# Performance work log

Measured on AMD Instinct MI355X. Metric: run time of the kernel, lower is better.

Reference implementation:

```python
import jax, jax.numpy as jnp
import numpy as np

SLOT_DIM = 64
EPS_SHIFT = 1e-6


def _mlp(x, Ws, bs):
    for i in range(len(Ws) - 1):
        x = jax.nn.relu(x @ Ws[i] + bs[i])
    return x @ Ws[-1] + bs[-1]


def setup_inputs() -> dict:
    key = jax.random.key(0)
    ks = jax.random.split(key, 16)
    B, C, H, W = 2, 64, 64, 64
    Q = 65536  # 256x256 output queries
    feat = jax.random.normal(ks[0], (B, C, H, W), jnp.float32)
    coord = jax.random.uniform(ks[1], (B, Q, 2), jnp.float32, -1.0, 1.0)
    cell = jnp.full((B, Q, 2), 2.0 / 256.0, jnp.float32)
    in_dim = C * 9 + 2 + 2  # unfolded feat + rel_coord + rel_cell
    dims = [in_dim, 256, 256, 256, 256, 3]
    params = {}
    for i in range(5):
        params[f"W{i}"] = jax.random.normal(ks[2 + i], (dims[i], dims[i + 1]), jnp.float32) * (1.0 / np.sqrt(dims[i]))
        params[f"b{i}"] = jnp.zeros((dims[i + 1],), jnp.float32)
    return {"feat": feat, "coord": coord, "cell": cell, **params}


def reference(feat, coord, cell, W0, b0, W1, b1, W2, b2, W3, b3, W4, b4):
    Ws = [W0, W1, W2, W3, W4]
    bs = [b0, b1, b2, b3, b4]
    B, C, H, W = feat.shape
    slot_flat = feat[:, -SLOT_DIM:].reshape(B, SLOT_DIM, H * W)
    # F.unfold(feat, 3, padding=1): channel order c*9 + ky*3 + kx
    pad = jnp.pad(feat, ((0, 0), (0, 0), (1, 1), (1, 1)))
    feat_unf = jnp.stack(
        [pad[:, :, ky:ky + H, kx:kx + W] for ky in range(3) for kx in range(3)],
        axis=2).reshape(B, C * 9, H * W)
    rx = 1.0 / H  # 2/H/2
    ry = 1.0 / W
    preds, slots = [], []
    for vx in (-1.0, 1.0):
        for vy in (-1.0, 1.0):
            cy = jnp.clip(coord[..., 0] + vx * rx + EPS_SHIFT, -1 + 1e-6, 1 - 1e-6)
            cx = jnp.clip(coord[..., 1] + vy * ry + EPS_SHIFT, -1 + 1e-6, 1 - 1e-6)
            # nearest grid_sample, align_corners=False: pix = (c+1)*N/2 - 0.5
            iy = jnp.clip(jnp.round((cy + 1.0) * H / 2.0 - 0.5), 0, H - 1).astype(jnp.int32)
            ix = jnp.clip(jnp.round((cx + 1.0) * W / 2.0 - 0.5), 0, W - 1).astype(jnp.int32)
            idx = iy * W + ix  # [B, Q]
            q_feat = jnp.take_along_axis(feat_unf, idx[:, None, :], axis=2).transpose(0, 2, 1)  # [B,Q,C*9]
            q_slot = jnp.take_along_axis(slot_flat, idx[:, None, :], axis=2).transpose(0, 2, 1)  # [B,Q,S]
            # make_coord pixel centers at sampled indices
            qc_y = -1.0 + (2.0 * iy.astype(coord.dtype) + 1.0) / H
            qc_x = -1.0 + (2.0 * ix.astype(coord.dtype) + 1.0) / W
            rel_y = (coord[..., 0] - qc_y) * H
            rel_x = (coord[..., 1] - qc_x) * W
            rel_cell = cell * jnp.asarray([H, W], coord.dtype)
            inp = jnp.concatenate([q_feat, rel_y[..., None], rel_x[..., None], rel_cell], axis=-1)
            preds.append(_mlp(inp, Ws, bs))  # [B,Q,3]
            slots.append(q_slot)
    # self-attention ensemble weighting
    slots = jnp.stack(slots, axis=-1)  # [B,Q,S,4]
    normed = slots / jnp.linalg.norm(slots, axis=-2, keepdims=True)
    n_shift = slots.shape[-1]
    attn = jnp.einsum('bqsi,bqsj->bqij', normed, normed) / SLOT_DIM  # mean over slot dim
    mask = 1.0 - jnp.eye(n_shift, dtype=attn.dtype)
    w = jnp.mean(attn * mask[None, None], axis=-1)  # [B,Q,4]
    w = w / jnp.sum(w, axis=-1, keepdims=True)
    ret = preds[0] * w[..., 0:1]
    for i in range(1, n_shift):
        ret = ret + preds[i] * w[..., i:i + 1]
    return ret
```

## Files before the change

### kernel.cpp

```cpp
#include <hip/hip_runtime.h>
#include <hip/hip_bf16.h>
#include <hip/hip_fp16.h>

typedef _Float16 f16x8 __attribute__((ext_vector_type(8)));
typedef _Float16 h2 __attribute__((ext_vector_type(2)));
typedef float f32x4 __attribute__((ext_vector_type(4)));

#define OFF_FEAT_T   0u
#define OFF_FEAT_H   (2u*1024*1024)
#define OFF_G        (3u*1024*1024)
#define OFF_WP1      (7u*1024*1024)
#define OFF_WP2      (OFF_WP1 + 131072u)
#define OFF_WP3      (OFF_WP2 + 131072u)
#define OFF_WP4      (OFF_WP3 + 131072u)
#define OFF_W0PT     (OFF_WP4 + 8192u)
#define OFF_W0E      (OFF_W0PT + 294912u)

__device__ __forceinline__ unsigned short f2h(float v) {
  return __builtin_bit_cast(unsigned short, (_Float16)v);
}
__device__ __forceinline__ unsigned pk2(float a, float b) {
  auto p = __builtin_amdgcn_cvt_pkrtz(a, b);
  return __builtin_bit_cast(unsigned, p);
}
__device__ __forceinline__ void block_sync() {
  asm volatile("s_waitcnt lgkmcnt(0)" ::: "memory");
  __builtin_amdgcn_s_barrier();
}

__global__ __launch_bounds__(256) void prep_kernel(
    const float* __restrict__ feat, const float* __restrict__ W0,
    const float* __restrict__ b0,
    const float* __restrict__ W1, const float* __restrict__ W2,
    const float* __restrict__ W3, const float* __restrict__ W4,
    char* __restrict__ ws)
{
  int flat = blockIdx.x * 256 + threadIdx.x;
  if (flat < 524288) {
    int c = flat & 63, x = (flat >> 6) & 63, y = (flat >> 12) & 63, b = flat >> 18;
    float f = feat[(((b*64 + c) << 6) + y)*64 + x];
    ((float*)(ws + OFF_FEAT_T))[flat] = f;
    ((unsigned short*)(ws + OFF_FEAT_H))[flat] = f2h(f);
    return;
  }
  int e = flat - 524288;
  if (e >= 44544) return;
  unsigned short o[8];
  char* dst;
  if (e < 24576) {
    int layer = e >> 13, ee = e & 8191;
    const float* Wsrc = layer == 0 ? W1 : (layer == 1 ? W2 : W3);
    int lane = ee & 63, nb = (ee >> 6) & 15, kk = ee >> 10;
    int n = nb*16 + (lane & 15), kb = kk*32 + ((lane >> 4) << 3);
    #pragma unroll
    for (int j = 0; j < 8; ++j) o[j] = f2h(Wsrc[(kb + j)*256 + n]);
    dst = ws + OFF_WP1 + layer*131072 + ee*16;
  } else if (e < 25088) {
    int ee = e - 24576;
    int lane = ee & 63, kk = ee >> 6;
    int n = lane & 15, kb = kk*32 + ((lane >> 4) << 3);
    #pragma unroll
    for (int j = 0; j < 8; ++j)
      o[j] = (n < 3) ? f2h(W4[(kb + j)*3 + n]) : (unsigned short)0;
    dst = ws + OFF_WP4 + ee*16;
  } else if (e < 43520) {
    int ee = e - 25088;
    int lane = ee & 63, nb = (ee >> 6) & 15, kk = ee >> 10;
    int n = nb*16 + (lane & 15), kb = kk*32 + ((lane >> 4) << 3);
    #pragma unroll
    for (int j = 0; j < 8; ++j) {
      int kp = kb + j, tap = kp >> 6, ch = kp & 63;
      o[j] = f2h(W0[(ch*9 + tap)*256 + n]);
    }
    dst = ws + OFF_W0PT + ee*16;
  } else {
    int ee = e - 43520;
    int lane = ee & 63, nb = ee >> 6;
    int n = nb*16 + (lane & 15), kb = (lane >> 4) << 3;
    #pragma unroll
    for (int j = 0; j < 8; ++j) {
      int k = kb + j;
      float v = (k < 4) ? W0[(576 + k)*256 + n] : (k == 4 ? b0[n] : 0.0f);
      o[j] = f2h(v);
    }
    dst = ws + OFF_W0E + ee*16;
  }
  uint4 v;
  v.x = (unsigned)o[0] | ((unsigned)o[1] << 16);
  v.y = (unsigned)o[2] | ((unsigned)o[3] << 16);
  v.z = (unsigned)o[4] | ((unsigned)o[5] << 16);
  v.w = (unsigned)o[6] | ((unsigned)o[7] << 16);
  *(uint4*)dst = v;
}

__global__ __launch_bounds__(256) void g_kernel(char* __restrict__ ws)
{
  __shared__ __align__(16) char As[32 * 1152];
  int t = threadIdx.x, lane = t & 63, w = t >> 6;
  int bid = blockIdx.x, b = bid >> 7, rb = bid & 127;
  int y = rb >> 1, x0 = (rb & 1) << 5;
  {
    int r = t >> 3, cq = t & 7;
    const unsigned short* fh = (const unsigned short*)(ws + OFF_FEAT_H);
    #pragma unroll
    for (int tap = 0; tap < 9; ++tap) {
      int dy = tap/3 - 1, dx = tap%3 - 1;
      int sy = y + dy, sx = x0 + r + dx;
      uint4 v = {0,0,0,0};
      if (sy >= 0 && sy < 64 && sx >= 0 && sx < 64)
        v = *(const uint4*)(fh + (((((b << 6) + sy) << 6) + sx) << 6) + (cq << 3));
      *(uint4*)(As + r*1152 + ((tap*128 + cq*16) ^ ((r & 7) << 4))) = v;
    }
  }
  __syncthreads();
  const f32x4 vzero = {0.f, 0.f, 0.f, 0.f};
  f32x4 acc[4][2];
  #pragma unroll
  for (int i = 0; i < 4; ++i)
    #pragma unroll
    for (int j = 0; j < 2; ++j) acc[i][j] = vzero;
  const unsigned short* wp0 = (const unsigned short*)(ws + OFF_W0PT);
  int lr = lane & 15, lg = lane >> 4;
  #pragma unroll
  for (int kk = 0; kk < 18; ++kk) {
    f16x8 a[4], bf[2];
    #pragma unroll
    for (int mf = 0; mf < 4; ++mf)
      a[mf] = *(const f16x8*)(wp0 + (((kk*16 + w*4 + mf)*64 + lane) << 3));
    #pragma unroll
    for (int nf = 0; nf < 2; ++nf) {
      int row = nf*16 + lr;
      bf[nf] = *(const f16x8*)(As + row*1152 + ((kk*64 + (lg << 4)) ^ ((row & 7) << 4)));
    }
    #pragma unroll
    for (int mf = 0; mf < 4; ++mf)
      #pragma unroll
      for (int nf = 0; nf < 2; ++nf)
        acc[mf][nf] = __builtin_amdgcn_mfma_f32_16x16x32_f16(a[mf], bf[nf], acc[mf][nf], 0, 0, 0);
  }
  unsigned short* gp = (unsigned short*)(ws + OFF_G);
  #pragma unroll
  for (int mf = 0; mf < 4; ++mf)
    #pragma unroll
    for (int nf = 0; nf < 2; ++nf) {
      int col = (w << 6) + mf*16 + (lg << 2);
      int p = (y << 6) + x0 + nf*16 + lr;
      uint2 ov;
      ov.x = pk2(acc[mf][nf][0], acc[mf][nf][1]);
      ov.y = pk2(acc[mf][nf][2], acc[mf][nf][3]);
      *(uint2*)(gp + ((((b << 12) + p) << 8) + col)) = ov;
    }
}

__device__ __forceinline__ void hidden_layer(const char* src, char* dst,
                                             const unsigned short* wp,
                                             const float* bias,
                                             int lane, int wc,
                                             const f16x8* apre)
{
  int lr = lane & 15, lg = lane >> 4;
  f32x4 acc[4][4];
  #pragma unroll
  for (int mf = 0; mf < 4; ++mf) {
    float4 bv = *(const float4*)(bias + (wc << 6) + (mf << 4) + (lg << 2));
    f32x4 bi = {bv.x, bv.y, bv.z, bv.w};
    #pragma unroll
    for (int nf = 0; nf < 4; ++nf) acc[mf][nf] = bi;
  }
  #pragma unroll
  for (int kk = 0; kk < 8; ++kk) {
    f16x8 a[4], bb[4];
    #pragma unroll
    for (int mf = 0; mf < 4; ++mf)
      a[mf] = (kk == 0) ? apre[mf]
            : *(const f16x8*)(wp + (((kk*16 + wc*4 + mf)*64 + lane) << 3));
    #pragma unroll
    for (int nf = 0; nf < 4; ++nf) {
      int row = (nf << 4) + lr;
      bb[nf] = *(const f16x8*)(src + row*512 + ((((kk << 2) + lg) ^ (row & 31)) << 4));
    }
    #pragma unroll
    for (int mf = 0; mf < 4; ++mf)
      #pragma unroll
      for (int nf = 0; nf < 4; ++nf)
        acc[mf][nf] = __builtin_amdgcn_mfma_f32_16x16x32_f16(a[mf], bb[nf], acc[mf][nf], 0, 0, 0);
  }
  #pragma unroll
  for (int mf = 0; mf < 4; ++mf) {
    int unit = (wc << 3) + (mf << 1) + (lg >> 1);
    int half8 = (lg & 1) << 3;
    #pragma unroll
    for (int nf = 0; nf < 4; ++nf) {
      int row = (nf << 4) + lr;
      float v0 = fmaxf(acc[mf][nf][0], 0.f);
      float v1 = fmaxf(acc[mf][nf][1], 0.f);
      float v2 = fmaxf(acc[mf][nf][2], 0.f);
      float v3 = fmaxf(acc[mf][nf][3], 0.f);
      uint2 ov;
      ov.x = pk2(v0, v1);
      ov.y = pk2(v2, v3);
      *(uint2*)(dst + row*512 + (((unit ^ (row & 31)) << 4) + half8)) = ov;
    }
  }
}

__global__ __launch_bounds__(256) void main_kernel(
    const float* __restrict__ coord, const float* __restrict__ cell,
    const float* __restrict__ b1, const float* __restrict__ b2,
    const float* __restrict__ b3, const float* __restrict__ b4,
    const char* __restrict__ ws, float* __restrict__ out)
{
  __shared__ __align__(16) char bufA[64*512];
  __shared__ __align__(16) char bufB[64*512];
  __shared__ __align__(16) float rel4[64][4];
  __shared__ int prow[64];
  __shared__ float preds[64][4];
  __shared__ float dots[16][12];

  int t = threadIdx.x, lane = t & 63, w = t >> 6;
  int lr = lane & 15, lg = lane >> 4;
  int bid = blockIdx.x, b = bid >> 12, qt = bid & 4095;
  int qbase = qt << 4;

  f16x8 a0[4];
  {
    const unsigned short* w0e = (const unsigned short*)(ws + OFF_W0E);
    #pragma unroll
    for (int mf = 0; mf < 4; ++mf)
      a0[mf] = *(const f16x8*)(w0e + (((w*4 + mf)*64 + lane) << 3));
  }
  if (t < 64) {
    int r = t, ql = r >> 2, s = r & 3;
    int gq = (b << 16) + qbase + ql;
    float c0 = coord[gq*2], c1 = coord[gq*2 + 1];
    float ce0 = cell[gq*2], ce1 = cell[gq*2 + 1];
    float vx = (s & 2) ? 1.0f : -1.0f;
    float vy = (s & 1) ? 1.0f : -1.0f;
    float cy = fminf(fmaxf(c0 + vx*(1.0f/64.0f) + 1e-6f, -1.0f + 1e-6f), 1.0f - 1e-6f);
    float cx = fminf(fmaxf(c1 + vy*(1.0f/64.0f) + 1e-6f, -1.0f + 1e-6f), 1.0f - 1e-6f);
    int iy = (int)fminf(fmaxf(rintf((cy + 1.0f)*32.0f - 0.5f), 0.0f), 63.0f);
    int ix = (int)fminf(fmaxf(rintf((cx + 1.0f)*32.0f - 0.5f), 0.0f), 63.0f);
    prow[r] = (iy << 6) + ix;
    float qcy = -1.0f + (float)(2*iy + 1)*(1.0f/64.0f);
    float qcx = -1.0f + (float)(2*ix + 1)*(1.0f/64.0f);
    rel4[r][0] = (c0 - qcy)*64.0f;
    rel4[r][1] = (c1 - qcx)*64.0f;
    rel4[r][2] = ce0*64.0f;
    rel4[r][3] = ce1*64.0f;
  }
  block_sync();
  {
    f16x8 bb0[4];
    int pr[4];
    #pragma unroll
    for (int nf = 0; nf < 4; ++nf) {
      int row = (nf << 4) + lr;
      float4 rv = *(const float4*)rel4[row];
      pr[nf] = prow[row];
      f16x8 v;
      v[0] = (_Float16)rv.x; v[1] = (_Float16)rv.y;
      v[2] = (_Float16)rv.z; v[3] = (_Float16)rv.w;
      v[4] = (_Float16)1.0f; v[5] = (_Float16)0.0f;
      v[6] = (_Float16)0.0f; v[7] = (_Float16)0.0f;
      bb0[nf] = v;
    }
    const unsigned short* gtab = (const unsigned short*)(ws + OFF_G);
    uint2 gg[4][4];
    #pragma unroll
    for (int nf = 0; nf < 4; ++nf) {
      const unsigned short* gpn = gtab + (((b << 12) + pr[nf]) << 8) + (w << 6) + (lg << 2);
      #pragma unroll
      for (int mf = 0; mf < 4; ++mf)
        gg[mf][nf] = *(const uint2*)(gpn + (mf << 4));
    }
    const f32x4 vzero = {0.f, 0.f, 0.f, 0.f};
    f32x4 acc[4][4];
    #pragma unroll
    for (int mf = 0; mf < 4; ++mf)
      #pragma unroll
      for (int nf = 0; nf < 4; ++nf)
        acc[mf][nf] = __builtin_amdgcn_mfma_f32_16x16x32_f16(a0[mf], bb0[nf], vzero, 0, 0, 0);
    const h2 z2 = {(_Float16)0.0f, (_Float16)0.0f};
    #pragma unroll
    for (int mf = 0; mf < 4; ++mf) {
      int unit = (w << 3) + (mf << 1) + (lg >> 1);
      int half8 = (lg & 1) << 3;
      #pragma unroll
      for (int nf = 0; nf < 4; ++nf) {
        int row = (nf << 4) + lr;
        h2 p0 = __builtin_bit_cast(h2, pk2(acc[mf][nf][0], acc[mf][nf][1]));
        h2 p1 = __builtin_bit_cast(h2, pk2(acc[mf][nf][2], acc[mf][nf][3]));
        h2 g0 = __builtin_bit_cast(h2, gg[mf][nf].x);
        h2 g1 = __builtin_bit_cast(h2, gg[mf][nf].y);
        h2 h0 = __builtin_elementwise_max(p0 + g0, z2);
        h2 h1 = __builtin_elementwise_max(p1 + g1, z2);
        uint2 ov;
        ov.x = __builtin_bit_cast(unsigned, h0);
        ov.y = __builtin_bit_cast(unsigned, h1);
        *(uint2*)(bufA + row*512 + (((unit ^ (row & 31)) << 4) + half8)) = ov;
      }
    }
  }
  const unsigned short* wp1 = (const unsigned short*)(ws + OFF_WP1);
  const unsigned short* wp2 = (const unsigned short*)(ws + OFF_WP2);
  const unsigned short* wp3 = (const unsigned short*)(ws + OFF_WP3);
  f16x8 ap[4];
  #pragma unroll
  for (int mf = 0; mf < 4; ++mf)
    ap[mf] = *(const f16x8*)(wp1 + (((w*4 + mf)*64 + lane) << 3));
  block_sync();
  hidden_layer(bufA, bufB, wp1, b1, lane, w, ap);
  #pragma unroll
  for (int mf = 0; mf < 4; ++mf)
    ap[mf] = *(const f16x8*)(wp2 + (((w*4 + mf)*64 + lane) << 3));
  block_sync();
  hidden_layer(bufB, bufA, wp2, b2, lane, w, ap);
  #pragma unroll
  for (int mf = 0; mf < 4; ++mf)
    ap[mf] = *(const f16x8*)(wp3 + (((w*4 + mf)*64 + lane) << 3));
  block_sync();
  hidden_layer(bufA, bufB, wp3, b3, lane, w, ap);
  block_sync();
  {
    const unsigned short* wp4 = (const unsigned short*)(ws + OFF_WP4);
    const f32x4 vzero = {0.f, 0.f, 0.f, 0.f};
    f32x4 acc = vzero;
    int row = (w << 4) + lr;
    #pragma unroll
    for (int kk = 0; kk < 8; ++kk) {
      f16x8 a = *(const f16x8*)(wp4 + ((kk*64 + lane) << 3));
      f16x8 bb = *(const f16x8*)(bufB + row*512 + ((((kk << 2) + lg) ^ (row & 31)) << 4));
      acc = __builtin_amdgcn_mfma_f32_16x16x32_f16(a, bb, acc, 0, 0, 0);
    }
    if (lg == 0) {
      #pragma unroll
      for (int ch = 0; ch < 3; ++ch) preds[row][ch] = acc[ch] + b4[ch];
    }
  }
  {
    int r = t >> 2, q4 = t & 3;
    const float* sp = (const float*)(ws + OFF_FEAT_T)
                    + (((b << 12) + prow[r]) << 6) + (q4 << 4);
    float* Sld = (float*)bufA;
    #pragma unroll
    for (int i = 0; i < 4; ++i)
      *(float4*)(Sld + r*76 + (q4 << 4) + (i << 2)) = *(const float4*)(sp + (i << 2));
  }
  block_sync();
  if (t < 160) {
    const int ia[10] = {0,1,2,3, 0,0,0,1,1,2};
    const int ib[10] = {0,1,2,3, 1,2,3,2,3,3};
    int q = t / 10, item = t - q*10;
    const float* Sld = (const float*)bufA;
    const float* ra = Sld + (q*4 + ia[item])*76;
    const float* rb = Sld + (q*4 + ib[item])*76;
    float s = 0.0f;
    #pragma unroll
    for (int i = 0; i < 16; ++i) {
      float4 va = *(const float4*)(ra + (i << 2));
      float4 vb = *(const float4*)(rb + (i << 2));
      s += va.x*vb.x + va.y*vb.y + va.z*vb.z + va.w*vb.w;
    }
    dots[q][item] = s;
  }
  block_sync();
  if (t < 16) {
    int q = t;
    float inv[4];
    #pragma unroll
    for (int i = 0; i < 4; ++i) inv[i] = 1.0f / sqrtf(dots[q][i]);
    const int pa[6] = {0,0,0,1,1,2};
    const int pb[6] = {1,2,3,2,3,3};
    float wgt[4] = {0.f, 0.f, 0.f, 0.f};
    #pragma unroll
    for (int pi = 0; pi < 6; ++pi) {
      float cij = dots[q][4 + pi]*inv[pa[pi]]*inv[pb[pi]];
      wgt[pa[pi]] += cij;
      wgt[pb[pi]] += cij;
    }
    float wsum = wgt[0] + wgt[1] + wgt[2] + wgt[3];
    float invw = 1.0f / wsum;
    size_t obase = (size_t)((b << 16) + qbase + q)*3;
    #pragma unroll
    for (int cch = 0; cch < 3; ++cch) {
      float v = preds[q*4 + 0][cch]*wgt[0] + preds[q*4 + 1][cch]*wgt[1]
              + preds[q*4 + 2][cch]*wgt[2] + preds[q*4 + 3][cch]*wgt[3];
      out[obase + cch] = v*invw;
    }
  }
}

extern "C" void kernel_launch(void* const* d_in, const int* in_sizes, int n_in,
                              void* d_out, int out_size, void* d_ws, size_t ws_size,
                              hipStream_t stream) {
  const float* feat  = (const float*)d_in[0];
  const float* coord = (const float*)d_in[1];
  const float* cell  = (const float*)d_in[2];
  const float* W0 = (const float*)d_in[3];
  const float* b0 = (const float*)d_in[4];
  const float* W1 = (const float*)d_in[5];
  const float* b1 = (const float*)d_in[6];
  const float* W2 = (const float*)d_in[7];
  const float* b2 = (const float*)d_in[8];
  const float* W3 = (const float*)d_in[9];
  const float* b3 = (const float*)d_in[10];
  const float* W4 = (const float*)d_in[11];
  const float* b4 = (const float*)d_in[12];
  char* ws = (char*)d_ws;
  float* out = (float*)d_out;
  prep_kernel<<<2222, 256, 0, stream>>>(feat, W0, b0, W1, W2, W3, W4, ws);
  g_kernel<<<256, 256, 0, stream>>>(ws);
  main_kernel<<<8192, 256, 0, stream>>>(coord, cell, b1, b2, b3, b4, ws, out);
}
```

Measured before the change: 366.6 us.

## Use a single in-place LDS activation buffer and raise occupancy to four blocks

Replaces the ping-pong bufA/bufB LDS activation buffers with one 32KB buffer that each hidden layer updates in place, adding a block barrier between the MFMA reads and the activation writes. It also drops the register prefetch of the first weight fragments, defers loading the layer-0 weights until after the coordinate setup, and adds a launch-bounds hint of 4 blocks per CU. The aim is to roughly halve LDS use and cut register pressure so more blocks fit per CU and latency is better hidden. In exchange it adds one extra barrier per layer plus one before the slot staging, and loses the overlap from prefetching weights.

```diff
diff --git a/kernel.cpp b/kernel.cpp
--- a/kernel.cpp
+++ b/kernel.cpp
@@ -152,11 +152,10 @@
     }
 }
 
-__device__ __forceinline__ void hidden_layer(const char* src, char* dst,
+__device__ __forceinline__ void hidden_layer(char* buf,
                                              const unsigned short* wp,
                                              const float* bias,
-                                             int lane, int wc,
-                                             const f16x8* apre)
+                                             int lane, int wc)
 {
   int lr = lane & 15, lg = lane >> 4;
   f32x4 acc[4][4];
@@ -172,12 +171,11 @@
     f16x8 a[4], bb[4];
     #pragma unroll
     for (int mf = 0; mf < 4; ++mf)
-      a[mf] = (kk == 0) ? apre[mf]
-            : *(const f16x8*)(wp + (((kk*16 + wc*4 + mf)*64 + lane) << 3));
+      a[mf] = *(const f16x8*)(wp + (((kk*16 + wc*4 + mf)*64 + lane) << 3));
     #pragma unroll
     for (int nf = 0; nf < 4; ++nf) {
       int row = (nf << 4) + lr;
-      bb[nf] = *(const f16x8*)(src + row*512 + ((((kk << 2) + lg) ^ (row & 31)) << 4));
+      bb[nf] = *(const f16x8*)(buf + row*512 + ((((kk << 2) + lg) ^ (row & 31)) << 4));
     }
     #pragma unroll
     for (int mf = 0; mf < 4; ++mf)
@@ -185,6 +183,7 @@
       for (int nf = 0; nf < 4; ++nf)
         acc[mf][nf] = __builtin_amdgcn_mfma_f32_16x16x32_f16(a[mf], bb[nf], acc[mf][nf], 0, 0, 0);
   }
+  block_sync();
   #pragma unroll
   for (int mf = 0; mf < 4; ++mf) {
     int unit = (wc << 3) + (mf << 1) + (lg >> 1);
@@ -199,19 +198,18 @@
       uint2 ov;
       ov.x = pk2(v0, v1);
       ov.y = pk2(v2, v3);
-      *(uint2*)(dst + row*512 + (((unit ^ (row & 31)) << 4) + half8)) = ov;
-    }
-  }
-}
-
-__global__ __launch_bounds__(256) void main_kernel(
+      *(uint2*)(buf + row*512 + (((unit ^ (row & 31)) << 4) + half8)) = ov;
+    }
+  }
+}
+
+__global__ __launch_bounds__(256, 4) void main_kernel(
     const float* __restrict__ coord, const float* __restrict__ cell,
     const float* __restrict__ b1, const float* __restrict__ b2,
     const float* __restrict__ b3, const float* __restrict__ b4,
     const char* __restrict__ ws, float* __restrict__ out)
 {
-  __shared__ __align__(16) char bufA[64*512];
-  __shared__ __align__(16) char bufB[64*512];
+  __shared__ __align__(16) char buf[64*512];
   __shared__ __align__(16) float rel4[64][4];
   __shared__ int prow[64];
   __shared__ float preds[64][4];
@@ -222,13 +220,6 @@
   int bid = blockIdx.x, b = bid >> 12, qt = bid & 4095;
   int qbase = qt << 4;
 
-  f16x8 a0[4];
-  {
-    const unsigned short* w0e = (const unsigned short*)(ws + OFF_W0E);
-    #pragma unroll
-    for (int mf = 0; mf < 4; ++mf)
-      a0[mf] = *(const f16x8*)(w0e + (((w*4 + mf)*64 + lane) << 3));
-  }
   if (t < 64) {
     int r = t, ql = r >> 2, s = r & 3;
     int gq = (b << 16) + qbase + ql;
@@ -250,6 +241,11 @@
   }
   block_sync();
   {
+    f16x8 a0[4];
+    const unsigned short* w0e = (const unsigned short*)(ws + OFF_W0E);
+    #pragma unroll
+    for (int mf = 0; mf < 4; ++mf)
+      a0[mf] = *(const f16x8*)(w0e + (((w*4 + mf)*64 + lane) << 3));
     f16x8 bb0[4];
     int pr[4];
     #pragma unroll
@@ -297,29 +293,16 @@
         uint2 ov;
         ov.x = __builtin_bit_cast(unsigned, h0);
         ov.y = __builtin_bit_cast(unsigned, h1);
-        *(uint2*)(bufA + row*512 + (((unit ^ (row & 31)) << 4) + half8)) = ov;
+        *(uint2*)(buf + row*512 + (((unit ^ (row & 31)) << 4) + half8)) = ov;
       }
     }
   }
-  const unsigned short* wp1 = (const unsigned short*)(ws + OFF_WP1);
-  const unsigned short* wp2 = (const unsigned short*)(ws + OFF_WP2);
-  const unsigned short* wp3 = (const unsigned short*)(ws + OFF_WP3);
-  f16x8 ap[4];
-  #pragma unroll
-  for (int mf = 0; mf < 4; ++mf)
-    ap[mf] = *(const f16x8*)(wp1 + (((w*4 + mf)*64 + lane) << 3));
-  block_sync();
-  hidden_layer(bufA, bufB, wp1, b1, lane, w, ap);
-  #pragma unroll
-  for (int mf = 0; mf < 4; ++mf)
-    ap[mf] = *(const f16x8*)(wp2 + (((w*4 + mf)*64 + lane) << 3));
-  block_sync();
-  hidden_layer(bufB, bufA, wp2, b2, lane, w, ap);
-  #pragma unroll
-  for (int mf = 0; mf < 4; ++mf)
-    ap[mf] = *(const f16x8*)(wp3 + (((w*4 + mf)*64 + lane) << 3));
-  block_sync();
-  hidden_layer(bufA, bufB, wp3, b3, lane, w, ap);
+  block_sync();
+  hidden_layer(buf, (const unsigned short*)(ws + OFF_WP1), b1, lane, w);
+  block_sync();
+  hidden_layer(buf, (const unsigned short*)(ws + OFF_WP2), b2, lane, w);
+  block_sync();
+  hidden_layer(buf, (const unsigned short*)(ws + OFF_WP3), b3, lane, w);
   block_sync();
   {
     const unsigned short* wp4 = (const unsigned short*)(ws + OFF_WP4);
@@ -329,7 +312,7 @@
     #pragma unroll
     for (int kk = 0; kk < 8; ++kk) {
       f16x8 a = *(const f16x8*)(wp4 + ((kk*64 + lane) << 3));
-      f16x8 bb = *(const f16x8*)(bufB + row*512 + ((((kk << 2) + lg) ^ (row & 31)) << 4));
+      f16x8 bb = *(const f16x8*)(buf + row*512 + ((((kk << 2) + lg) ^ (row & 31)) << 4));
       acc = __builtin_amdgcn_mfma_f32_16x16x32_f16(a, bb, acc, 0, 0, 0);
     }
     if (lg == 0) {
@@ -337,11 +320,12 @@
       for (int ch = 0; ch < 3; ++ch) preds[row][ch] = acc[ch] + b4[ch];
     }
   }
+  block_sync();
   {
     int r = t >> 2, q4 = t & 3;
     const float* sp = (const float*)(ws + OFF_FEAT_T)
                     + (((b << 12) + prow[r]) << 6) + (q4 << 4);
-    float* Sld = (float*)bufA;
+    float* Sld = (float*)buf;
     #pragma unroll
     for (int i = 0; i < 4; ++i)
       *(float4*)(Sld + r*76 + (q4 << 4) + (i << 2)) = *(const float4*)(sp + (i << 2));
@@ -351,7 +335,7 @@
     const int ia[10] = {0,1,2,3, 0,0,0,1,1,2};
     const int ib[10] = {0,1,2,3, 1,2,3,2,3,3};
     int q = t / 10, item = t - q*10;
-    const float* Sld = (const float*)bufA;
+    const float* Sld = (const float*)buf;
     const float* ra = Sld + (q*4 + ia[item])*76;
     const float* rb = Sld + (q*4 + ib[item])*76;
     float s = 0.0f;
```

Result: slower. 617.4 us (+68.4%).

## Split MLP layers across eight waves per block instead of four

Applied to the files above, without the earlier changes.

The main kernel now launches 512 threads per block, and each of the eight waves computes 32 output units per layer instead of 64. This halves per-wave accumulator and weight registers. The final-layer projection and the slot-feature staging now run concurrently on separate wave groups. It also drops the prefetching of first-k-slice weights across barriers, trading that overlap for more waves and lower register pressure per wave.

```diff
diff --git a/kernel.cpp b/kernel.cpp
--- a/kernel.cpp
+++ b/kernel.cpp
@@ -155,39 +155,37 @@
 __device__ __forceinline__ void hidden_layer(const char* src, char* dst,
                                              const unsigned short* wp,
                                              const float* bias,
-                                             int lane, int wc,
-                                             const f16x8* apre)
+                                             int lane, int w)
 {
   int lr = lane & 15, lg = lane >> 4;
-  f32x4 acc[4][4];
-  #pragma unroll
-  for (int mf = 0; mf < 4; ++mf) {
-    float4 bv = *(const float4*)(bias + (wc << 6) + (mf << 4) + (lg << 2));
+  f32x4 acc[2][4];
+  #pragma unroll
+  for (int mf = 0; mf < 2; ++mf) {
+    float4 bv = *(const float4*)(bias + (w << 5) + (mf << 4) + (lg << 2));
     f32x4 bi = {bv.x, bv.y, bv.z, bv.w};
     #pragma unroll
     for (int nf = 0; nf < 4; ++nf) acc[mf][nf] = bi;
   }
   #pragma unroll
   for (int kk = 0; kk < 8; ++kk) {
-    f16x8 a[4], bb[4];
-    #pragma unroll
-    for (int mf = 0; mf < 4; ++mf)
-      a[mf] = (kk == 0) ? apre[mf]
-            : *(const f16x8*)(wp + (((kk*16 + wc*4 + mf)*64 + lane) << 3));
+    f16x8 a[2], bb[4];
+    #pragma unroll
+    for (int mf = 0; mf < 2; ++mf)
+      a[mf] = *(const f16x8*)(wp + (((kk*16 + w*2 + mf)*64 + lane) << 3));
     #pragma unroll
     for (int nf = 0; nf < 4; ++nf) {
       int row = (nf << 4) + lr;
       bb[nf] = *(const f16x8*)(src + row*512 + ((((kk << 2) + lg) ^ (row & 31)) << 4));
     }
     #pragma unroll
-    for (int mf = 0; mf < 4; ++mf)
+    for (int mf = 0; mf < 2; ++mf)
       #pragma unroll
       for (int nf = 0; nf < 4; ++nf)
         acc[mf][nf] = __builtin_amdgcn_mfma_f32_16x16x32_f16(a[mf], bb[nf], acc[mf][nf], 0, 0, 0);
   }
   #pragma unroll
-  for (int mf = 0; mf < 4; ++mf) {
-    int unit = (wc << 3) + (mf << 1) + (lg >> 1);
+  for (int mf = 0; mf < 2; ++mf) {
+    int unit = (w << 2) + (mf << 1) + (lg >> 1);
     int half8 = (lg & 1) << 3;
     #pragma unroll
     for (int nf = 0; nf < 4; ++nf) {
@@ -204,7 +202,7 @@
   }
 }
 
-__global__ __launch_bounds__(256) void main_kernel(
+__global__ __launch_bounds__(512) void main_kernel(
     const float* __restrict__ coord, const float* __restrict__ cell,
     const float* __restrict__ b1, const float* __restrict__ b2,
     const float* __restrict__ b3, const float* __restrict__ b4,
@@ -222,13 +220,6 @@
   int bid = blockIdx.x, b = bid >> 12, qt = bid & 4095;
   int qbase = qt << 4;
 
-  f16x8 a0[4];
-  {
-    const unsigned short* w0e = (const unsigned short*)(ws + OFF_W0E);
-    #pragma unroll
-    for (int mf = 0; mf < 4; ++mf)
-      a0[mf] = *(const f16x8*)(w0e + (((w*4 + mf)*64 + lane) << 3));
-  }
   if (t < 64) {
     int r = t, ql = r >> 2, s = r & 3;
     int gq = (b << 16) + qbase + ql;
@@ -250,6 +241,11 @@
   }
   block_sync();
   {
+    f16x8 a0[2];
+    const unsigned short* w0e = (const unsigned short*)(ws + OFF_W0E);
+    #pragma unroll
+    for (int mf = 0; mf < 2; ++mf)
+      a0[mf] = *(const f16x8*)(w0e + (((w*2 + mf)*64 + lane) << 3));
     f16x8 bb0[4];
     int pr[4];
     #pragma unroll
@@ -265,25 +261,25 @@
       bb0[nf] = v;
     }
     const unsigned short* gtab = (const unsigned short*)(ws + OFF_G);
-    uint2 gg[4][4];
+    uint2 gg[2][4];
     #pragma unroll
     for (int nf = 0; nf < 4; ++nf) {
-      const unsigned short* gpn = gtab + (((b << 12) + pr[nf]) << 8) + (w << 6) + (lg << 2);
-      #pragma unroll
-      for (int mf = 0; mf < 4; ++mf)
+      const unsigned short* gpn = gtab + (((b << 12) + pr[nf]) << 8) + (w << 5) + (lg << 2);
+      #pragma unroll
+      for (int mf = 0; mf < 2; ++mf)
         gg[mf][nf] = *(const uint2*)(gpn + (mf << 4));
     }
     const f32x4 vzero = {0.f, 0.f, 0.f, 0.f};
-    f32x4 acc[4][4];
-    #pragma unroll
-    for (int mf = 0; mf < 4; ++mf)
+    f32x4 acc[2][4];
+    #pragma unroll
+    for (int mf = 0; mf < 2; ++mf)
       #pragma unroll
       for (int nf = 0; nf < 4; ++nf)
         acc[mf][nf] = __builtin_amdgcn_mfma_f32_16x16x32_f16(a0[mf], bb0[nf], vzero, 0, 0, 0);
     const h2 z2 = {(_Float16)0.0f, (_Float16)0.0f};
     #pragma unroll
-    for (int mf = 0; mf < 4; ++mf) {
-      int unit = (w << 3) + (mf << 1) + (lg >> 1);
+    for (int mf = 0; mf < 2; ++mf) {
+      int unit = (w << 2) + (mf << 1) + (lg >> 1);
       int half8 = (lg & 1) << 3;
       #pragma unroll
       for (int nf = 0; nf < 4; ++nf) {
@@ -301,27 +297,14 @@
       }
     }
   }
-  const unsigned short* wp1 = (const unsigned short*)(ws + OFF_WP1);
-  const unsigned short* wp2 = (const unsigned short*)(ws + OFF_WP2);
-  const unsigned short* wp3 = (const unsigned short*)(ws + OFF_WP3);
-  f16x8 ap[4];
-  #pragma unroll
-  for (int mf = 0; mf < 4; ++mf)
-    ap[mf] = *(const f16x8*)(wp1 + (((w*4 + mf)*64 + lane) << 3));
-  block_sync();
-  hidden_layer(bufA, bufB, wp1, b1, lane, w, ap);
-  #pragma unroll
-  for (int mf = 0; mf < 4; ++mf)
-    ap[mf] = *(const f16x8*)(wp2 + (((w*4 + mf)*64 + lane) << 3));
-  block_sync();
-  hidden_layer(bufB, bufA, wp2, b2, lane, w, ap);
-  #pragma unroll
-  for (int mf = 0; mf < 4; ++mf)
-    ap[mf] = *(const f16x8*)(wp3 + (((w*4 + mf)*64 + lane) << 3));
-  block_sync();
-  hidden_layer(bufA, bufB, wp3, b3, lane, w, ap);
-  block_sync();
-  {
+  block_sync();
+  hidden_layer(bufA, bufB, (const unsigned short*)(ws + OFF_WP1), b1, lane, w);
+  block_sync();
+  hidden_layer(bufB, bufA, (const unsigned short*)(ws + OFF_WP2), b2, lane, w);
+  block_sync();
+  hidden_layer(bufA, bufB, (const unsigned short*)(ws + OFF_WP3), b3, lane, w);
+  block_sync();
+  if (w < 4) {
     const unsigned short* wp4 = (const unsigned short*)(ws + OFF_WP4);
     const f32x4 vzero = {0.f, 0.f, 0.f, 0.f};
     f32x4 acc = vzero;
@@ -336,9 +319,9 @@
       #pragma unroll
       for (int ch = 0; ch < 3; ++ch) preds[row][ch] = acc[ch] + b4[ch];
     }
-  }
-  {
-    int r = t >> 2, q4 = t & 3;
+  } else {
+    int tt = t - 256;
+    int r = tt >> 2, q4 = tt & 3;
     const float* sp = (const float*)(ws + OFF_FEAT_T)
                     + (((b << 12) + prow[r]) << 6) + (q4 << 4);
     float* Sld = (float*)bufA;
@@ -410,5 +393,5 @@
   float* out = (float*)d_out;
   prep_kernel<<<2222, 256, 0, stream>>>(feat, W0, b0, W1, W2, W3, W4, ws);
   g_kernel<<<256, 256, 0, stream>>>(ws);
-  main_kernel<<<8192, 256, 0, stream>>>(coord, cell, b1, b2, b3, b4, ws, out);
-}
+  main_kernel<<<8192, 512, 0, stream>>>(coord, cell, b1, b2, b3, b4, ws, out);
+}
```

New measurement: 406.2 us. 10.8% more time.
